# Optimization experiments

Measured on AMD Instinct MI355X. Metric: run time of the kernel, lower is better.

The kernel has to match this reference:

```python
import jax, jax.numpy as jnp
import numpy as np

B, T, H, O = 128, 256, 512, 256  # batch, max_seq, hidden_length, output_token_length
X = O + H  # GRU cell input size (concat of y and attention context)


def _glorot(key, shape):
    fan_in, fan_out = shape[0], shape[1]
    limit = np.sqrt(6.0 / (fan_in + fan_out))
    return jax.random.uniform(key, shape, jnp.float32, -limit, limit)


def setup_inputs() -> dict:
    key = jax.random.key(0)
    ks = jax.random.split(key, 16)
    return {
        "h": jax.random.normal(ks[0], (B, T, H), jnp.float32),
        "s0": jax.random.normal(ks[1], (B, H), jnp.float32),
        # y_dense: Dense(H,tanh) -> Dense(H,tanh) -> Dense(O,linear)
        "Wy1": _glorot(ks[2], (H, H)), "by1": jnp.zeros((H,), jnp.float32),
        "Wy2": _glorot(ks[3], (H, H)), "by2": jnp.zeros((H,), jnp.float32),
        "Wy3": _glorot(ks[4], (H, O)), "by3": jnp.zeros((O,), jnp.float32),
        # e_dense: Dense(H,tanh) on concat([h_i, s]) (2H) -> Dense(1,linear)
        "We1": _glorot(ks[5], (2 * H, H)), "be1": jnp.zeros((H,), jnp.float32),
        "We2": _glorot(ks[6], (H, 1)), "be2": jnp.zeros((1,), jnp.float32),
        # GRU cell weights
        "Wxr": _glorot(ks[7], (X, H)), "Whr": _glorot(ks[8], (H, H)), "br": jnp.zeros((H,), jnp.float32),
        "Wxu": _glorot(ks[9], (X, H)), "Whu": _glorot(ks[10], (H, H)), "bu": jnp.zeros((H,), jnp.float32),
        "Wxh": _glorot(ks[11], (X, H)), "Whh": _glorot(ks[12], (H, H)),
    }


def reference(h, s0, Wy1, by1, Wy2, by2, Wy3, by3, We1, be1, We2, be2,
              Wxr, Whr, br, Wxu, Whu, bu, Wxh, Whh):
    We1_h, We1_s = We1[:H], We1[H:]
    # Precompute encoder-side attention projection once: [B, T, H]
    h_proj = jnp.einsum('bth,hk->btk', h, We1_h)

    def step(s, _):
        # output head (uses state BEFORE update, matching original)
        y = jnp.tanh(s @ Wy1 + by1)
        y = jnp.tanh(y @ Wy2 + by2)
        y = y @ Wy3 + by3  # [B, O]
        # Bahdanau attention over all T encoder positions (vectorized)
        s_proj = s @ We1_s + be1  # [B, H]
        e = jnp.squeeze(jnp.tanh(h_proj + s_proj[:, None, :]) @ We2, -1) + be2[0]  # [B, T]
        a = jax.nn.softmax(e, axis=-1)
        c = jnp.einsum('bt,bth->bh', a, h)  # [B, H]
        # GRU cell on concat([y, c])
        x = jnp.concatenate([y, c], axis=-1)  # [B, O+H]
        r = jax.nn.sigmoid(x @ Wxr + s @ Whr + br)
        u = jax.nn.sigmoid(x @ Wxu + s @ Whu + bu)
        h_cand = jnp.tanh(x @ Wxh + (r * s) @ Whh)
        s_new = (1.0 - u) * h_cand + u * s
        return s_new, y

    _, ys = jax.lax.scan(step, s0, None, length=T)  # ys: [T, B, O]
    return jnp.transpose(ys, (1, 0, 2))  # [B, T, O]
```

## Files before the change

kernel.cpp:

```cpp
#include <hip/hip_runtime.h>

#define B_ 128
#define T_ 256
#define H_ 512
#define O_ 256
#define X_ 768

typedef unsigned short u16;
typedef unsigned int u32;

#if __has_builtin(__builtin_amdgcn_exp2f)
#define EXP2(x) __builtin_amdgcn_exp2f(x)
#else
#define EXP2(x) exp2f(x)
#endif
#if __has_builtin(__builtin_amdgcn_rcpf)
#define RCPF(x) __builtin_amdgcn_rcpf(x)
#else
#define RCPF(x) (1.0f / (x))
#endif

#define LOG2E_F 1.4426950408889634f
#define TWOLOG2E_F 2.8853900817779268f

typedef __attribute__((ext_vector_type(8))) short short8;
typedef __attribute__((ext_vector_type(4))) float f32x4;

__device__ __forceinline__ float bf2f(u16 v) {
  union { u32 u; float f; } c; c.u = ((u32)v) << 16; return c.f;
}
__device__ __forceinline__ u16 f2bf(float f) {
  union { float f; u32 u; } c; c.f = f;
  return (u16)((c.u + 0x7FFFu + ((c.u >> 16) & 1u)) >> 16);
}
__device__ __forceinline__ float ftanh(float x) {
  x = fminf(fmaxf(x, -40.f), 40.f);
  float z = EXP2(x * TWOLOG2E_F);
  return (z - 1.0f) * RCPF(z + 1.0f);
}
__device__ __forceinline__ float fsigm(float x) {
  x = fminf(fmaxf(x, -40.f), 40.f);
  return RCPF(1.0f + EXP2(-x * LOG2E_F));
}

__device__ u16 g_hp[(size_t)B_ * T_ * H_];
__device__ u16 g_hb[(size_t)B_ * T_ * H_];
__device__ float g_s[B_ * H_];
__device__ float g_u[B_ * H_];
__device__ float g_sp[B_ * H_];
__device__ float g_p[B_ * H_];

__device__ float g_wcru[512 * 1024];
__device__ float g_wch[512 * 512];
__device__ float g_bru[1024];
__device__ float g_bh[512];

__device__ u16 g_ah[(size_t)8 * 96 * 512];
__device__ u16 g_al[(size_t)8 * 96 * 512];

__device__ u16 Wy1p[(size_t)32 * 16 * 512];
__device__ u16 Wy2p[(size_t)32 * 16 * 512];
__device__ u16 Wy3p[(size_t)16 * 16 * 512];
__device__ u16 We1sp[(size_t)32 * 16 * 512];
__device__ u16 WRUp[(size_t)64 * 48 * 512];
__device__ u16 WPp[(size_t)32 * 32 * 512];
__device__ u16 Whhp[(size_t)32 * 16 * 512];

__device__ u16 cby1[H_];
__device__ u16 cby2[H_];
__device__ u16 cby3[O_];
__device__ u16 cbe1[H_];
__device__ u16 cWe2[H_];

__device__ __forceinline__ void store_packed(int b, int col, float v) {
  u16 hi = f2bf(v);
  size_t idx = (((size_t)(b >> 4) * 96 + (col >> 5)) << 9) +
               ((((col >> 3) & 3) * 16 + (b & 15)) << 3) + (col & 7);
  g_ah[idx] = hi;
  g_al[idx] = f2bf(v - bf2f(hi));
}

#define DEF_CONV(NAME, ARR, N)                                     \
  __global__ void conv_##NAME(const float* __restrict__ s) {       \
    int i = blockIdx.x * 256 + threadIdx.x;                        \
    if (i < (N)) ARR[i] = f2bf(s[i]);                              \
  }

DEF_CONV(by1, cby1, H_)
DEF_CONV(by2, cby2, H_)
DEF_CONV(by3, cby3, O_)
DEF_CONV(be1, cbe1, H_)
DEF_CONV(We2, cWe2, H_)

__global__ void conv_h(const float* __restrict__ s) {
  size_t i = (size_t)blockIdx.x * 256 + threadIdx.x;
  g_hb[i] = f2bf(s[i]);
}

template <int MODE>
__global__ void __launch_bounds__(256) fgemm_comp(const float* __restrict__ A,
                                                  const float* __restrict__ B) {
  float* C = (MODE == 0) ? g_wcru : (MODE == 1) ? (g_wcru + 512) : g_wch;
  const int ldc = (MODE == 2) ? 512 : 1024;
  __shared__ float Ast[32][72];
  __shared__ float Bs[32][72];
  const int tid = threadIdx.x;
  const int tx = tid & 15, ty = tid >> 4;
  const int n0 = blockIdx.x << 6;
  const int m0 = blockIdx.y << 6;
  float acc[4][4] = {};
  for (int k0 = 0; k0 < 256; k0 += 32) {
    {
      int row = tid >> 2, kq = (tid & 3) << 3;
      const float* src = A + (size_t)(m0 + row) * 256 + k0 + kq;
      float4 v0 = *(const float4*)src;
      float4 v1 = *(const float4*)(src + 4);
      Ast[kq + 0][row] = v0.x; Ast[kq + 1][row] = v0.y;
      Ast[kq + 2][row] = v0.z; Ast[kq + 3][row] = v0.w;
      Ast[kq + 4][row] = v1.x; Ast[kq + 5][row] = v1.y;
      Ast[kq + 6][row] = v1.z; Ast[kq + 7][row] = v1.w;
    }
    {
      int kr = tid >> 3, nq = (tid & 7) << 3;
      const float* src = B + (size_t)(k0 + kr) * 512 + n0 + nq;
      float4 v0 = *(const float4*)src;
      float4 v1 = *(const float4*)(src + 4);
      float* d = &Bs[kr][nq];
      d[0] = v0.x; d[1] = v0.y; d[2] = v0.z; d[3] = v0.w;
      d[4] = v1.x; d[5] = v1.y; d[6] = v1.z; d[7] = v1.w;
    }
    __syncthreads();
#pragma unroll
    for (int kk = 0; kk < 32; ++kk) {
      const float4 a4 = *(const float4*)&Ast[kk][ty << 2];
      const float4 b4 = *(const float4*)&Bs[kk][tx << 2];
      float av[4] = {a4.x, a4.y, a4.z, a4.w};
      float bv[4] = {b4.x, b4.y, b4.z, b4.w};
#pragma unroll
      for (int i = 0; i < 4; ++i)
#pragma unroll
        for (int j = 0; j < 4; ++j) acc[i][j] = fmaf(av[i], bv[j], acc[i][j]);
    }
    __syncthreads();
  }
#pragma unroll
  for (int i = 0; i < 4; ++i)
#pragma unroll
    for (int j = 0; j < 4; ++j)
      C[(size_t)(m0 + ty * 4 + i) * ldc + n0 + tx * 4 + j] = acc[i][j];
}

__global__ void bias_fold(const float* __restrict__ by3,
                          const float* __restrict__ Wxr,
                          const float* __restrict__ Wxu,
                          const float* __restrict__ br,
                          const float* __restrict__ bu,
                          const float* __restrict__ Wxh) {
  int n = blockIdx.x * 256 + threadIdx.x;
  if (n < 1024) {
    const float* W = (n < 512) ? Wxr : Wxu;
    int nn = n & 511;
    float acc = (n < 512) ? br[nn] : bu[nn];
    for (int k = 0; k < 256; ++k) acc += by3[k] * W[(size_t)k * 512 + nn];
    g_bru[n] = acc;
  } else if (n < 1536) {
    int nn = n - 1024;
    float acc = 0.f;
    for (int k = 0; k < 256; ++k) acc += by3[k] * Wxh[(size_t)k * 512 + nn];
    g_bh[nn] = acc;
  }
}

#define DEF_PACKB(NAME, DST, NKT, SRCEXPR)                               \
  __global__ void NAME(const float* __restrict__ S0) {                   \
    int gid = blockIdx.x * 256 + threadIdx.x;                            \
    int l = gid & 63, kt = (gid >> 6) % (NKT);                           \
    int ntile = gid / (64 * (NKT));                                      \
    int n = ntile * 16 + (l & 15);                                       \
    __align__(16) u16 tmp[8];                                            \
    _Pragma("unroll")                                                    \
    for (int j = 0; j < 8; ++j) {                                        \
      int k = kt * 32 + ((l >> 4) << 3) + j;                             \
      tmp[j] = f2bf(SRCEXPR);                                            \
    }                                                                    \
    *(uint4*)(DST + (size_t)gid * 8) = *(const uint4*)tmp;               \
  }

DEF_PACKB(pack_Wy1, Wy1p, 16, S0[(size_t)k * 512 + n])
DEF_PACKB(pack_Wy2, Wy2p, 16, S0[(size_t)k * 512 + n])
DEF_PACKB(pack_Wy3, Wy3p, 16, S0[(size_t)k * 256 + n])
DEF_PACKB(pack_We1s, We1sp, 16, S0[(size_t)(512 + k) * 512 + n])

__global__ void pack_WRU(const float* __restrict__ Wxr, const float* __restrict__ Whr,
                         const float* __restrict__ Wxu, const float* __restrict__ Whu) {
  int gid = blockIdx.x * 256 + threadIdx.x;
  int l = gid & 63, kt = (gid >> 6) % 48;
  int ntile = gid / (64 * 48);
  int n = ntile * 16 + (l & 15);
  int nn = n & 511;
  __align__(16) u16 tmp[8];
#pragma unroll
  for (int j = 0; j < 8; ++j) {
    int k = kt * 32 + ((l >> 4) << 3) + j;
    float v;
    if (k < 512) v = g_wcru[(size_t)k * 1024 + n];
    else if (k < 1024) {
      v = (n < 512) ? Wxr[(size_t)(k - 512 + 256) * 512 + nn]
                    : Wxu[(size_t)(k - 512 + 256) * 512 + nn];
    } else {
      v = (n < 512) ? Whr[(size_t)(k - 1024) * 512 + nn]
                    : Whu[(size_t)(k - 1024) * 512 + nn];
    }
    tmp[j] = f2bf(v);
  }
  *(uint4*)(WRUp + (size_t)gid * 8) = *(const uint4*)tmp;
}

__global__ void pack_WP(const float* __restrict__ Wxh) {
  int gid = blockIdx.x * 256 + threadIdx.x;
  int l = gid & 63, kt = (gid >> 6) & 31;
  int ntile = gid >> 11;
  int n = ntile * 16 + (l & 15);
  __align__(16) u16 tmp[8];
#pragma unroll
  for (int j = 0; j < 8; ++j) {
    int k = kt * 32 + ((l >> 4) << 3) + j;
    float v;
    if (k < 512) v = g_wch[(size_t)k * 512 + n];
    else v = Wxh[(size_t)(k - 512 + 256) * 512 + n];
    tmp[j] = f2bf(v);
  }
  *(uint4*)(WPp + (size_t)gid * 8) = *(const uint4*)tmp;
}

__global__ void pack_Whh(const float* __restrict__ Whh) {
  int gid = blockIdx.x * 256 + threadIdx.x;
  int l = gid & 63, kt = (gid >> 6) & 15;
  int ntile = gid >> 10;
  int n = ntile * 16 + (l & 15);
  __align__(16) u16 tmp[8];
#pragma unroll
  for (int j = 0; j < 8; ++j) {
    int k = kt * 32 + ((l >> 4) << 3) + j;
    tmp[j] = f2bf(Whh[(size_t)k * 512 + n]);
  }
  *(uint4*)(Whhp + (size_t)gid * 8) = *(const uint4*)tmp;
}

__global__ void init_kernel(const float* __restrict__ s0) {
  int g = blockIdx.x * blockDim.x + threadIdx.x;
  if (g < B_ * H_) {
    float v = s0[g];
    g_s[g] = v;
    int b = g >> 9, n = g & 511;
    store_packed(b, 1024 + n, v);
  }
}

__global__ void __launch_bounds__(256) hproj_kernel(const float* __restrict__ hh,
                                                    const float* __restrict__ We1) {
  __shared__ float Ast[32][72];
  __shared__ float Bs[32][72];
  const int tid = threadIdx.x;
  const int tx = tid & 15, ty = tid >> 4;
  const int n0 = blockIdx.x << 6;
  const int m0 = blockIdx.y << 6;
  float acc[4][4] = {};
  for (int k0 = 0; k0 < H_; k0 += 32) {
    {
      int row = tid >> 2, kq = (tid & 3) << 3;
      const float* src = hh + (size_t)(m0 + row) * H_ + k0 + kq;
      float4 v0 = *(const float4*)src;
      float4 v1 = *(const float4*)(src + 4);
      Ast[kq + 0][row] = v0.x; Ast[kq + 1][row] = v0.y;
      Ast[kq + 2][row] = v0.z; Ast[kq + 3][row] = v0.w;
      Ast[kq + 4][row] = v1.x; Ast[kq + 5][row] = v1.y;
      Ast[kq + 6][row] = v1.z; Ast[kq + 7][row] = v1.w;
    }
    {
      int kr = tid >> 3, nq = (tid & 7) << 3;
      const float* src = We1 + (size_t)(k0 + kr) * H_ + n0 + nq;
      float4 v0 = *(const float4*)src;
      float4 v1 = *(const float4*)(src + 4);
      float* d = &Bs[kr][nq];
      d[0] = v0.x; d[1] = v0.y; d[2] = v0.z; d[3] = v0.w;
      d[4] = v1.x; d[5] = v1.y; d[6] = v1.z; d[7] = v1.w;
    }
    __syncthreads();
#pragma unroll
    for (int kk = 0; kk < 32; ++kk) {
      const float4 a4 = *(const float4*)&Ast[kk][ty << 2];
      const float4 b4 = *(const float4*)&Bs[kk][tx << 2];
      float av[4] = {a4.x, a4.y, a4.z, a4.w};
      float bv[4] = {b4.x, b4.y, b4.z, b4.w};
#pragma unroll
      for (int i = 0; i < 4; ++i)
#pragma unroll
        for (int j = 0; j < 4; ++j) acc[i][j] = fmaf(av[i], bv[j], acc[i][j]);
    }
    __syncthreads();
  }
#pragma unroll
  for (int i = 0; i < 4; ++i) {
    u16* dst = g_hp + (size_t)(m0 + ty * 4 + i) * H_ + n0 + tx * 4;
    u32 w0 = (u32)f2bf(acc[i][0]) | ((u32)f2bf(acc[i][1]) << 16);
    u32 w1 = (u32)f2bf(acc[i][2]) | ((u32)f2bf(acc[i][3]) << 16);
    *(u32*)dst = w0;
    *(u32*)(dst + 2) = w1;
  }
}

#define FMA8(pk, sk, A)                                          \
  {                                                              \
    u32 ww0 = pk.x, ww1 = pk.y, ww2 = pk.z, ww3 = pk.w;          \
    A[0] = fmaf(sk, bf2f((u16)(ww0 & 0xffffu)), A[0]);           \
    A[1] = fmaf(sk, bf2f((u16)(ww0 >> 16)), A[1]);               \
    A[2] = fmaf(sk, bf2f((u16)(ww1 & 0xffffu)), A[2]);           \
    A[3] = fmaf(sk, bf2f((u16)(ww1 >> 16)), A[3]);               \
    A[4] = fmaf(sk, bf2f((u16)(ww2 & 0xffffu)), A[4]);           \
    A[5] = fmaf(sk, bf2f((u16)(ww2 >> 16)), A[5]);               \
    A[6] = fmaf(sk, bf2f((u16)(ww3 & 0xffffu)), A[6]);           \
    A[7] = fmaf(sk, bf2f((u16)(ww3 >> 16)), A[7]);               \
  }

template <int KTA0, int NKT_B, int KTW, int NW, int NT>
__device__ __forceinline__ void gemm_w(const u16* __restrict__ BP, int mt,
                                       int nbt, int tid, float* smem) {
  const int l = tid & 63, w = tid >> 6;
  f32x4 acc[NT];
#pragma unroll
  for (int nt = 0; nt < NT; ++nt) acc[nt] = (f32x4){0.f, 0.f, 0.f, 0.f};
  const size_t abase = (((size_t)mt * 96 + KTA0 + w * KTW) << 9) + l * 8;
#pragma unroll
  for (int kk = 0; kk < KTW; ++kk) {
    short8 ah = *(const short8*)(g_ah + abase + (size_t)kk * 512);
    short8 al = *(const short8*)(g_al + abase + (size_t)kk * 512);
    const size_t bbase =
        (((size_t)(nbt * NT) * NKT_B + w * KTW + kk) << 9) + l * 8;
#pragma unroll
    for (int nt = 0; nt < NT; ++nt) {
      short8 bb = *(const short8*)(BP + bbase + (((size_t)nt * NKT_B) << 9));
      acc[nt] = __builtin_amdgcn_mfma_f32_16x16x32_bf16(ah, bb, acc[nt], 0, 0, 0);
      acc[nt] = __builtin_amdgcn_mfma_f32_16x16x32_bf16(al, bb, acc[nt], 0, 0, 0);
    }
  }
  float* pw = smem + w * (NT * 256);
  const int r0 = (l >> 4) * 4, c0 = l & 15;
#pragma unroll
  for (int r = 0; r < 4; ++r)
#pragma unroll
    for (int nt = 0; nt < NT; ++nt)
      pw[(r0 + r) * (NT * 16) + nt * 16 + c0] = acc[nt][r];
  __syncthreads();
}

#define EPI_W(row, col, NW, NT)                                      \
  float v = 0.f;                                                     \
  _Pragma("unroll") for (int ww = 0; ww < (NW); ++ww)                \
      v += smem[ww * ((NT) * 256) + (row) * ((NT) * 16) + (col)];

__global__ void __launch_bounds__(1024) k1_y1sp() {
  __shared__ __align__(16) float smem[8192];
  const int tid = threadIdx.x;
  const int bid = blockIdx.x;
  if (bid < 128) {
    const int mt = bid >> 4, nbt = bid & 15;
    gemm_w<32, 16, 1, 16, 2>(Wy1p, mt, nbt, tid, smem);
    if (tid < 512) {
      int row = tid >> 5, col = tid & 31;
      EPI_W(row, col, 16, 2);
      int gb = mt * 16 + row, gc = nbt * 32 + col;
      v += bf2f(cby1[gc]);
      store_packed(gb, 2048 + gc, ftanh(v));
    }
  } else {
    const int blk2 = bid - 128;
    const int mt = blk2 >> 4, nbt = blk2 & 15;
    gemm_w<32, 16, 1, 16, 2>(We1sp, mt, nbt, tid, smem);
    if (tid < 512) {
      int row = tid >> 5, col = tid & 31;
      EPI_W(row, col, 16, 2);
      int gb = mt * 16 + row, gc = nbt * 32 + col;
      g_sp[gb * H_ + gc] = v + bf2f(cbe1[gc]);
    }
  }
}

__global__ void __launch_bounds__(1024) k2_y2attn() {
  __shared__ __align__(16) float smem[10240];
  __shared__ float red[32];
  const int tid = threadIdx.x;
  const int bid = blockIdx.x;
  if (bid < 128) {
    const int mt = bid >> 4, nbt = bid & 15;
    gemm_w<64, 16, 1, 16, 2>(Wy2p, mt, nbt, tid, smem);
    if (tid < 512) {
      int row = tid >> 5, col = tid & 31;
      EPI_W(row, col, 16, 2);
      int gb = mt * 16 + row, gc = nbt * 32 + col;
      v += bf2f(cby2[gc]);
      store_packed(gb, gc, ftanh(v));
    }
  } else {
    const int b = bid - 128;
    float* sm_e = smem + 1024;
    if (tid < 512) {
      float spv = g_sp[b * H_ + tid];
      float w2 = bf2f(cWe2[tid]);
      smem[2 * tid] = spv * TWOLOG2E_F;
      smem[2 * tid + 1] = -2.0f * w2;
    }
    __syncthreads();
    const int wv = tid >> 6, l = tid & 63;
    const int rr = l & 15, q = l >> 4;
    {
      int tp = wv * 16 + rr;
      const u16* rowp = g_hp + ((size_t)(b * T_ + tp) << 9);
      float part = 0.f;
      for (int i = 0; i < 16; ++i) {
        int c0 = i * 32 + q * 8;
        uint4 pk = *(const uint4*)(rowp + c0);
        const float4* swp = reinterpret_cast<const float4*>(smem + 2 * c0);
        float4 f0 = swp[0], f1 = swp[1], f2 = swp[2], f3 = swp[3];
        u32 ww[4] = {pk.x, pk.y, pk.z, pk.w};
        {
          float h0 = bf2f((u16)(ww[0] & 0xffffu)), h1 = bf2f((u16)(ww[0] >> 16));
          float x0 = fmaf(h0, TWOLOG2E_F, f0.x);
          float x1 = fmaf(h1, TWOLOG2E_F, f0.z);
          part = fmaf(f0.y, RCPF(EXP2(x0) + 1.f), part);
          part = fmaf(f0.w, RCPF(EXP2(x1) + 1.f), part);
        }
        {
          float h0 = bf2f((u16)(ww[1] & 0xffffu)), h1 = bf2f((u16)(ww[1] >> 16));
          float x0 = fmaf(h0, TWOLOG2E_F, f1.x);
          float x1 = fmaf(h1, TWOLOG2E_F, f1.z);
          part = fmaf(f1.y, RCPF(EXP2(x0) + 1.f), part);
          part = fmaf(f1.w, RCPF(EXP2(x1) + 1.f), part);
        }
        {
          float h0 = bf2f((u16)(ww[2] & 0xffffu)), h1 = bf2f((u16)(ww[2] >> 16));
          float x0 = fmaf(h0, TWOLOG2E_F, f2.x);
          float x1 = fmaf(h1, TWOLOG2E_F, f2.z);
          part = fmaf(f2.y, RCPF(EXP2(x0) + 1.f), part);
          part = fmaf(f2.w, RCPF(EXP2(x1) + 1.f), part);
        }
        {
          float h0 = bf2f((u16)(ww[3] & 0xffffu)), h1 = bf2f((u16)(ww[3] >> 16));
          float x0 = fmaf(h0, TWOLOG2E_F, f3.x);
          float x1 = fmaf(h1, TWOLOG2E_F, f3.z);
          part = fmaf(f3.y, RCPF(EXP2(x0) + 1.f), part);
          part = fmaf(f3.w, RCPF(EXP2(x1) + 1.f), part);
        }
      }
      part += __shfl_xor(part, 16, 64);
      part += __shfl_xor(part, 32, 64);
      if (q == 0) sm_e[tp] = part;
    }
    __syncthreads();
    float v = (tid < T_) ? sm_e[tid] : -3.0e38f;
    float m = v;
#pragma unroll
    for (int off = 32; off > 0; off >>= 1) m = fmaxf(m, __shfl_xor(m, off, 64));
    if (l == 0) red[wv] = m;
    __syncthreads();
    m = red[0];
#pragma unroll
    for (int rI = 1; rI < 16; ++rI) m = fmaxf(m, red[rI]);
    float pe = (tid < T_) ? EXP2((v - m) * LOG2E_F) : 0.f;
    float ssum = pe;
#pragma unroll
    for (int off = 32; off > 0; off >>= 1) ssum += __shfl_xor(ssum, off, 64);
    if (l == 0) red[16 + wv] = ssum;
    __syncthreads();
    float tot = 0.f;
#pragma unroll
    for (int rI = 0; rI < 16; ++rI) tot += red[16 + rI];
    float ainv = RCPF(tot);
    if (tid < T_) sm_e[tid] = pe * ainv;
    __syncthreads();
    {
      const int ts = tid >> 6, c = tid & 63, n0 = c << 3;
      float a[8] = {};
      for (int tp = ts * 16; tp < ts * 16 + 16; ++tp) {
        uint4 pk = *(const uint4*)(g_hb + ((size_t)(b * T_ + tp) << 9) + n0);
        float av = sm_e[tp];
        FMA8(pk, av, a);
      }
      float* pt = smem + 1536 + ts * 512 + n0;
#pragma unroll
      for (int j = 0; j < 8; ++j) pt[j] = a[j];
    }
    __syncthreads();
    if (tid < 512) {
      float v2 = 0.f;
#pragma unroll
      for (int kk = 0; kk < 16; ++kk) v2 += smem[1536 + kk * 512 + tid];
      store_packed(b, 512 + tid, v2);
    }
  }
}

__global__ void __launch_bounds__(1024) k3_y3rup(float* __restrict__ out, int t) {
  __shared__ __align__(16) float smem[16384];
  const int tid = threadIdx.x;
  const int bid = blockIdx.x;
  if (bid < 32) {
    const int mt3 = bid >> 2, nbt = bid & 3;
    gemm_w<0, 16, 1, 16, 4>(Wy3p, mt3, nbt, tid, smem);
    int row = tid >> 6, col = tid & 63;
    EPI_W(row, col, 16, 4);
    int gb = mt3 * 16 + row, gc = nbt * 64 + col;
    v += bf2f(cby3[gc]);
    out[((size_t)gb * T_ + t) * O_ + gc] = v;
  } else if (bid < 160) {
    const int idx2 = bid - 32;
    const int mt = idx2 >> 4, nbt = idx2 & 15;
    gemm_w<0, 48, 3, 16, 4>(WRUp, mt, nbt, tid, smem);
    int row = tid >> 6, col = tid & 63;
    EPI_W(row, col, 16, 4);
    int gb = mt * 16 + row, gc = nbt * 64 + col;
    v += g_bru[gc];
    if (gc < 512) {
      float rv = fsigm(v);
      float rs = rv * g_s[gb * H_ + gc];
      store_packed(gb, 1536 + gc, rs);
    } else {
      g_u[gb * H_ + (gc - 512)] = fsigm(v);
    }
  } else {
    const int idx2 = bid - 160;
    const int mt = idx2 >> 3, nbt = idx2 & 7;
    gemm_w<0, 32, 2, 16, 4>(WPp, mt, nbt, tid, smem);
    int row = tid >> 6, col = tid & 63;
    EPI_W(row, col, 16, 4);
    int gb = mt * 16 + row, gc = nbt * 64 + col;
    g_p[gb * H_ + gc] = v + g_bh[gc];
  }
}

__global__ void __launch_bounds__(1024) k4_hc() {
  __shared__ __align__(16) float smem[8192];
  const int tid = threadIdx.x;
  const int bid = blockIdx.x;
  const int mt = bid >> 4, nbt = bid & 15;
  gemm_w<48, 16, 1, 16, 2>(Whhp, mt, nbt, tid, smem);
  if (tid < 512) {
    int row = tid >> 5, col = tid & 31;
    EPI_W(row, col, 16, 2);
    int gb = mt * 16 + row, gc = nbt * 32 + col;
    int sidx = gb * H_ + gc;
    v += g_p[sidx];
    float hc = ftanh(v);
    float uu = g_u[sidx];
    float sn = (1.f - uu) * hc + uu * g_s[sidx];
    g_s[sidx] = sn;
    store_packed(gb, 1024 + gc, sn);
  }
}

extern "C" void kernel_launch(void* const* d_in, const int* in_sizes, int n_in,
                              void* d_out, int out_size, void* d_ws, size_t ws_size,
                              hipStream_t stream) {
  (void)in_sizes; (void)n_in; (void)out_size; (void)d_ws; (void)ws_size;
  const float* h = (const float*)d_in[0];
  float* out = (float*)d_out;

#define CONV(NAME, IDX, N) \
  hipLaunchKernelGGL(conv_##NAME, dim3(((N) + 255) / 256), dim3(256), 0, stream, \
                     (const float*)d_in[IDX])
  CONV(by1, 3, H_);
  CONV(by2, 5, H_);
  CONV(by3, 7, O_);
  CONV(be1, 9, H_);
  CONV(We2, 10, H_);
#undef CONV
  hipLaunchKernelGGL((fgemm_comp<0>), dim3(8, 8), dim3(256), 0, stream,
                     (const float*)d_in[6], (const float*)d_in[12]);
  hipLaunchKernelGGL((fgemm_comp<1>), dim3(8, 8), dim3(256), 0, stream,
                     (const float*)d_in[6], (const float*)d_in[15]);
  hipLaunchKernelGGL((fgemm_comp<2>), dim3(8, 8), dim3(256), 0, stream,
                     (const float*)d_in[6], (const float*)d_in[18]);
  hipLaunchKernelGGL(bias_fold, dim3(6), dim3(256), 0, stream,
                     (const float*)d_in[7], (const float*)d_in[12],
                     (const float*)d_in[15], (const float*)d_in[14],
                     (const float*)d_in[17], (const float*)d_in[18]);
  hipLaunchKernelGGL(pack_Wy1, dim3(128), dim3(256), 0, stream, (const float*)d_in[2]);
  hipLaunchKernelGGL(pack_Wy2, dim3(128), dim3(256), 0, stream, (const float*)d_in[4]);
  hipLaunchKernelGGL(pack_Wy3, dim3(64), dim3(256), 0, stream, (const float*)d_in[6]);
  hipLaunchKernelGGL(pack_We1s, dim3(128), dim3(256), 0, stream, (const float*)d_in[8]);
  hipLaunchKernelGGL(pack_WRU, dim3(768), dim3(256), 0, stream,
                     (const float*)d_in[12], (const float*)d_in[13],
                     (const float*)d_in[15], (const float*)d_in[16]);
  hipLaunchKernelGGL(pack_WP, dim3(256), dim3(256), 0, stream,
                     (const float*)d_in[18]);
  hipLaunchKernelGGL(pack_Whh, dim3(128), dim3(256), 0, stream,
                     (const float*)d_in[19]);
  hipLaunchKernelGGL(conv_h, dim3((B_ * T_ * H_) / 256), dim3(256), 0, stream, h);
  hipLaunchKernelGGL(init_kernel, dim3(256), dim3(256), 0, stream,
                     (const float*)d_in[1]);
  hipLaunchKernelGGL(hproj_kernel, dim3(8, 512), dim3(256), 0, stream, h,
                     (const float*)d_in[8]);

  for (int t = 0; t < T_; ++t) {
    hipLaunchKernelGGL(k1_y1sp, dim3(256), dim3(1024), 0, stream);
    hipLaunchKernelGGL(k2_y2attn, dim3(256), dim3(1024), 0, stream);
    hipLaunchKernelGGL(k3_y3rup, dim3(224), dim3(1024), 0, stream, out, t);
    hipLaunchKernelGGL(k4_hc, dim3(128), dim3(1024), 0, stream);
  }
}
```

Baseline: 7.932 ms.

## Fuse candidate-state input GEMM into k4 with concatenated Wxh/Whh weights

The P = x·Wxh GEMM moves out of k3 and into k4_hc, where it becomes one GEMM over a concatenated K=1536 packed weight (W4p) covering the folded y path, the context, and r*s. This drops the g_p round trip through global memory and shrinks k3's grid. k4 now uses 16x16 output tiles with 256 blocks, each of 16 waves covering 3 k-tiles. The cost is more work on the serial critical path in k4, since the P computation no longer runs alongside the r/u GEMM in k3.

Measured after the change: 8.425 ms. +6.2%, slower.

```diff
diff --git a/kernel.cpp b/kernel.cpp
--- a/kernel.cpp
+++ b/kernel.cpp
@@ -48,7 +48,6 @@
 __device__ float g_s[B_ * H_];
 __device__ float g_u[B_ * H_];
 __device__ float g_sp[B_ * H_];
-__device__ float g_p[B_ * H_];
 
 __device__ float g_wcru[512 * 1024];
 __device__ float g_wch[512 * 512];
@@ -63,8 +62,7 @@
 __device__ u16 Wy3p[(size_t)16 * 16 * 512];
 __device__ u16 We1sp[(size_t)32 * 16 * 512];
 __device__ u16 WRUp[(size_t)64 * 48 * 512];
-__device__ u16 WPp[(size_t)32 * 32 * 512];
-__device__ u16 Whhp[(size_t)32 * 16 * 512];
+__device__ u16 W4p[(size_t)32 * 48 * 512];
 
 __device__ u16 cby1[H_];
 __device__ u16 cby2[H_];
@@ -216,10 +214,11 @@
   *(uint4*)(WRUp + (size_t)gid * 8) = *(const uint4*)tmp;
 }
 
-__global__ void pack_WP(const float* __restrict__ Wxh) {
+__global__ void pack_W4(const float* __restrict__ Wxh,
+                        const float* __restrict__ Whh) {
   int gid = blockIdx.x * 256 + threadIdx.x;
-  int l = gid & 63, kt = (gid >> 6) & 31;
-  int ntile = gid >> 11;
+  int l = gid & 63, kt = (gid >> 6) % 48;
+  int ntile = gid / (64 * 48);
   int n = ntile * 16 + (l & 15);
   __align__(16) u16 tmp[8];
 #pragma unroll
@@ -227,24 +226,11 @@
     int k = kt * 32 + ((l >> 4) << 3) + j;
     float v;
     if (k < 512) v = g_wch[(size_t)k * 512 + n];
-    else v = Wxh[(size_t)(k - 512 + 256) * 512 + n];
+    else if (k < 1024) v = Wxh[(size_t)(k - 512 + 256) * 512 + n];
+    else v = Whh[(size_t)(k - 1024) * 512 + n];
     tmp[j] = f2bf(v);
   }
-  *(uint4*)(WPp + (size_t)gid * 8) = *(const uint4*)tmp;
-}
-
-__global__ void pack_Whh(const float* __restrict__ Whh) {
-  int gid = blockIdx.x * 256 + threadIdx.x;
-  int l = gid & 63, kt = (gid >> 6) & 15;
-  int ntile = gid >> 10;
-  int n = ntile * 16 + (l & 15);
-  __align__(16) u16 tmp[8];
-#pragma unroll
-  for (int j = 0; j < 8; ++j) {
-    int k = kt * 32 + ((l >> 4) << 3) + j;
-    tmp[j] = f2bf(Whh[(size_t)k * 512 + n]);
-  }
-  *(uint4*)(Whhp + (size_t)gid * 8) = *(const uint4*)tmp;
+  *(uint4*)(W4p + (size_t)gid * 8) = *(const uint4*)tmp;
 }
 
 __global__ void init_kernel(const float* __restrict__ s0) {
@@ -351,6 +337,28 @@
 #pragma unroll
     for (int nt = 0; nt < NT; ++nt)
       pw[(r0 + r) * (NT * 16) + nt * 16 + c0] = acc[nt][r];
+  __syncthreads();
+}
+
+__device__ __forceinline__ void gemm_hc(int mt, int nbt, int tid, float* smem) {
+  const int l = tid & 63, w = tid >> 6;
+  f32x4 acc = {0.f, 0.f, 0.f, 0.f};
+#pragma unroll
+  for (int kk = 0; kk < 3; ++kk) {
+    int ktL = w * 3 + kk;
+    int ktA = (ktL < 32) ? ktL : (ktL + 16);
+    const size_t abase = (((size_t)mt * 96 + ktA) << 9) + l * 8;
+    short8 ah = *(const short8*)(g_ah + abase);
+    short8 al = *(const short8*)(g_al + abase);
+    const size_t bbase = (((size_t)nbt * 48 + ktL) << 9) + l * 8;
+    short8 bb = *(const short8*)(W4p + bbase);
+    acc = __builtin_amdgcn_mfma_f32_16x16x32_bf16(ah, bb, acc, 0, 0, 0);
+    acc = __builtin_amdgcn_mfma_f32_16x16x32_bf16(al, bb, acc, 0, 0, 0);
+  }
+  float* pw = smem + w * 256;
+  const int r0 = (l >> 4) * 4, c0 = l & 15;
+#pragma unroll
+  for (int r = 0; r < 4; ++r) pw[(r0 + r) * 16 + c0] = acc[r];
   __syncthreads();
 }
 
@@ -500,7 +508,7 @@
   }
 }
 
-__global__ void __launch_bounds__(1024) k3_y3rup(float* __restrict__ out, int t) {
+__global__ void __launch_bounds__(1024) k3_y3ru(float* __restrict__ out, int t) {
   __shared__ __align__(16) float smem[16384];
   const int tid = threadIdx.x;
   const int bid = blockIdx.x;
@@ -512,7 +520,7 @@
     int gb = mt3 * 16 + row, gc = nbt * 64 + col;
     v += bf2f(cby3[gc]);
     out[((size_t)gb * T_ + t) * O_ + gc] = v;
-  } else if (bid < 160) {
+  } else {
     const int idx2 = bid - 32;
     const int mt = idx2 >> 4, nbt = idx2 & 15;
     gemm_w<0, 48, 3, 16, 4>(WRUp, mt, nbt, tid, smem);
@@ -527,30 +535,23 @@
     } else {
       g_u[gb * H_ + (gc - 512)] = fsigm(v);
     }
-  } else {
-    const int idx2 = bid - 160;
-    const int mt = idx2 >> 3, nbt = idx2 & 7;
-    gemm_w<0, 32, 2, 16, 4>(WPp, mt, nbt, tid, smem);
-    int row = tid >> 6, col = tid & 63;
-    EPI_W(row, col, 16, 4);
-    int gb = mt * 16 + row, gc = nbt * 64 + col;
-    g_p[gb * H_ + gc] = v + g_bh[gc];
   }
 }
 
 __global__ void __launch_bounds__(1024) k4_hc() {
-  __shared__ __align__(16) float smem[8192];
+  __shared__ __align__(16) float smem[4096];
   const int tid = threadIdx.x;
   const int bid = blockIdx.x;
-  const int mt = bid >> 4, nbt = bid & 15;
-  gemm_w<48, 16, 1, 16, 2>(Whhp, mt, nbt, tid, smem);
-  if (tid < 512) {
-    int row = tid >> 5, col = tid & 31;
-    EPI_W(row, col, 16, 2);
-    int gb = mt * 16 + row, gc = nbt * 32 + col;
+  const int mt = bid >> 5, nbt = bid & 31;
+  gemm_hc(mt, nbt, tid, smem);
+  if (tid < 256) {
+    int row = tid >> 4, col = tid & 15;
+    float v = 0.f;
+#pragma unroll
+    for (int ww = 0; ww < 16; ++ww) v += smem[ww * 256 + row * 16 + col];
+    int gb = mt * 16 + row, gc = nbt * 16 + col;
     int sidx = gb * H_ + gc;
-    v += g_p[sidx];
-    float hc = ftanh(v);
+    float hc = ftanh(v + g_bh[gc]);
     float uu = g_u[sidx];
     float sn = (1.f - uu) * hc + uu * g_s[sidx];
     g_s[sidx] = sn;
@@ -591,10 +592,8 @@
   hipLaunchKernelGGL(pack_WRU, dim3(768), dim3(256), 0, stream,
                      (const float*)d_in[12], (const float*)d_in[13],
                      (const float*)d_in[15], (const float*)d_in[16]);
-  hipLaunchKernelGGL(pack_WP, dim3(256), dim3(256), 0, stream,
-                     (const float*)d_in[18]);
-  hipLaunchKernelGGL(pack_Whh, dim3(128), dim3(256), 0, stream,
-                     (const float*)d_in[19]);
+  hipLaunchKernelGGL(pack_W4, dim3(384), dim3(256), 0, stream,
+                     (const float*)d_in[18], (const float*)d_in[19]);
   hipLaunchKernelGGL(conv_h, dim3((B_ * T_ * H_) / 256), dim3(256), 0, stream, h);
   hipLaunchKernelGGL(init_kernel, dim3(256), dim3(256), 0, stream,
                      (const float*)d_in[1]);
@@ -604,7 +603,7 @@
   for (int t = 0; t < T_; ++t) {
     hipLaunchKernelGGL(k1_y1sp, dim3(256), dim3(1024), 0, stream);
     hipLaunchKernelGGL(k2_y2attn, dim3(256), dim3(1024), 0, stream);
-    hipLaunchKernelGGL(k3_y3rup, dim3(224), dim3(1024), 0, stream, out, t);
-    hipLaunchKernelGGL(k4_hc, dim3(128), dim3(1024), 0, stream);
-  }
-}
+    hipLaunchKernelGGL(k3_y3ru, dim3(160), dim3(1024), 0, stream, out, t);
+    hipLaunchKernelGGL(k4_hc, dim3(256), dim3(1024), 0, stream);
+  }
+}
```
